# Optimization experiments

Measured on AMD Instinct MI355X. Metric: run time of the kernel, lower is better.

The kernel has to match this reference:

```python
import jax, jax.numpy as jnp
import numpy as np
import math

B, S, D, H = 2, 2048, 1024, 16
HD = D // H  # head dim = 64


def setup_inputs() -> dict:
    key = jax.random.key(0)
    k1, k2, k3, k4, k5 = jax.random.split(key, 5)
    query = jax.random.normal(k1, (B, S, D), dtype=jnp.float32)
    # tail padding: sequence lengths 1536 and 1792 -> positions >= length are padded (True)
    lengths = jnp.array([1536, 1792], dtype=jnp.int32)
    padding_mask = jnp.arange(S, dtype=jnp.int32)[None, :] >= lengths[:, None]  # [B,S] bool
    qkv_w = jax.random.normal(k2, (3 * D, D), dtype=jnp.float32) * 0.02
    qkv_b = jax.random.uniform(k3, (3 * D,), dtype=jnp.float32, minval=-0.03, maxval=0.03)
    out_w = jax.random.normal(k4, (D, D), dtype=jnp.float32) * 0.02
    out_b = jax.random.uniform(k5, (D,), dtype=jnp.float32, minval=-0.03, maxval=0.03)
    return {"query": query, "padding_mask": padding_mask,
            "qkv_w": qkv_w, "qkv_b": qkv_b, "out_w": out_w, "out_b": out_b}


def reference(query, padding_mask, qkv_w, qkv_b, out_w, out_b):
    # self-attention path (qkv_same=True): fused qkv projection then split
    qkv = query @ qkv_w.T + qkv_b                      # [B,S,3D]
    q, k, v = jnp.split(qkv, 3, axis=-1)               # each [B,S,D]

    def split_heads(x):
        return x.reshape(B, S, H, HD).transpose(0, 2, 1, 3)  # [B,H,S,HD]

    q, k, v = split_heads(q), split_heads(k), split_heads(v)

    # scores scaled by sqrt(head_dim)
    w = jnp.einsum('bhqd,bhkd->bhqk', q, k) / math.sqrt(HD)  # [B,H,S,S]

    # causal (future) mask: strict upper triangle masked
    future = jnp.triu(jnp.ones((S, S), dtype=bool), 1)
    w = jnp.where(future[None, None, :, :], -jnp.inf, w)
    # key padding mask
    w = jnp.where(padding_mask[:, None, None, :], -jnp.inf, w)

    a = jax.nn.softmax(w, axis=-1)
    # rows of fully-padded sequences are zeroed (dropout is identity in eval)
    all_masked = jnp.all(padding_mask, axis=-1)        # [B]
    a = jnp.where(all_masked[:, None, None, None], 0.0, a)

    x = jnp.einsum('bhqk,bhkd->bhqd', a, v)            # [B,H,S,HD]
    x = x.transpose(0, 2, 1, 3).reshape(B, S, D)       # merge heads
    return x @ out_w.T + out_b
```

## Files before the change

kernel.cpp:

```cpp
#include <hip/hip_runtime.h>
#include <hip/hip_bf16.h>
#include <stdint.h>

#define S_  2048
#define B_  2
#define H_  16
#define D_  1024
#define HD_ 64

typedef short short8 __attribute__((ext_vector_type(8)));
typedef float f32x4  __attribute__((ext_vector_type(4)));
typedef float f32x16 __attribute__((ext_vector_type(16)));

__device__ __forceinline__ unsigned short bf16_rne(float f) {
  unsigned int u = __float_as_uint(f);
  u += 0x7fffu + ((u >> 16) & 1u);
  return (unsigned short)(u >> 16);
}

__device__ __forceinline__ f32x4 mfma_bf16(short8 a, short8 b, f32x4 c) {
  return __builtin_amdgcn_mfma_f32_16x16x32_bf16(a, b, c, 0, 0, 0);
}

__device__ __forceinline__ f32x16 mfma32(short8 a, short8 b, f32x16 c) {
  return __builtin_amdgcn_mfma_f32_32x32x16_bf16(a, b, c, 0, 0, 0);
}

__device__ __forceinline__ unsigned int cvtpk_bf16(float lo, float hi) {
  unsigned int r;
  asm("v_cvt_pk_bf16_f32 %0, %1, %2" : "=v"(r) : "v"(lo), "v"(hi));
  return r;
}

__global__ void cvt3_kernel(const float* __restrict__ a, unsigned short* __restrict__ oa, int na8,
                            const float* __restrict__ b, unsigned short* __restrict__ ob, int nb8,
                            const float* __restrict__ c, unsigned short* __restrict__ oc, int nc8) {
  int i = blockIdx.x * blockDim.x + threadIdx.x;
  const float* in; unsigned short* out; int idx;
  if (i < na8) { in = a; out = oa; idx = i; }
  else if (i < na8 + nb8) { in = b; out = ob; idx = i - na8; }
  else if (i < na8 + nb8 + nc8) { in = c; out = oc; idx = i - na8 - nb8; }
  else return;
  const float4* p = (const float4*)in + (size_t)idx * 2;
  float4 x = p[0], y = p[1];
  union { unsigned short u[8]; short8 v; } r;
  r.u[0] = bf16_rne(x.x); r.u[1] = bf16_rne(x.y);
  r.u[2] = bf16_rne(x.z); r.u[3] = bf16_rne(x.w);
  r.u[4] = bf16_rne(y.x); r.u[5] = bf16_rne(y.y);
  r.u[6] = bf16_rne(y.z); r.u[7] = bf16_rne(y.w);
  *((short8*)out + idx) = r.v;
}

__global__ void lengths_kernel(const void* __restrict__ mask, int* __restrict__ lens) {
  __shared__ int mn[B_];
  __shared__ int anyb;
  int t = threadIdx.x;
  if (t < B_) mn[t] = S_;
  if (t == 0) anyb = 0;
  __syncthreads();
  const unsigned char* mb = (const unsigned char*)mask;
  for (int i = t; i < B_ * S_; i += 256) {
    if (mb[i]) { anyb = 1; atomicMin(&mn[i >> 11], i & (S_ - 1)); }
  }
  __syncthreads();
  if (!anyb) {
    const int* mi = (const int*)mask;
    for (int i = t; i < B_ * S_; i += 256) {
      if (mi[i]) atomicMin(&mn[i >> 11], i & (S_ - 1));
    }
    __syncthreads();
  }
  if (t < B_) lens[t] = mn[t];
}

__global__ __launch_bounds__(512, 2) void gemm8p_kernel(
    const unsigned short* __restrict__ A,
    const unsigned short* __restrict__ W,
    int K, int NBX,
    const float* __restrict__ bias,
    unsigned short* __restrict__ qb,
    unsigned short* __restrict__ kb,
    unsigned short* __restrict__ vb) {
  __shared__ __align__(16) unsigned short lds[65536];

  const int nwg = gridDim.x;
  const int cpx = nwg >> 3;
  const int bid = blockIdx.x;
  const int virt = (bid & 7) * cpx + (bid >> 3);
  const int bx = virt % NBX, by = virt / NBX;
  const int tile_m = by * 256, tile_n = bx * 256;
  const int t = threadIdx.x;
  const int lane = t & 63, w = t >> 6;
  const int wm = w >> 2, wn = w & 3;
  const int l15 = lane & 15, lk = lane >> 4;
  const int NT = K >> 6;

  f32x4 acc[8][4];
#pragma unroll
  for (int i = 0; i < 8; i++)
#pragma unroll
    for (int j = 0; j < 4; j++) { f32x4 z = {0.f, 0.f, 0.f, 0.f}; acc[i][j] = z; }

  const int L0 = t, L1 = 512 + t;
  const int r0 = L0 >> 3, c0 = (L0 & 7) ^ (r0 & 7);
  const int r1 = L1 >> 3, c1 = (L1 & 7) ^ (r1 & 7);

#define STAGE_HALF(SRC, GROW0, DSTE, KC)                                      \
  {                                                                           \
    __builtin_amdgcn_global_load_lds(                                         \
        (const __attribute__((address_space(1))) void*)(                      \
            (SRC) + (size_t)((GROW0) + r0) * K + (KC) + c0 * 8),              \
        (__attribute__((address_space(3))) void*)(&lds[(DSTE) + L0 * 8]),     \
        16, 0, 0);                                                            \
    __builtin_amdgcn_global_load_lds(                                         \
        (const __attribute__((address_space(1))) void*)(                      \
            (SRC) + (size_t)((GROW0) + r1) * K + (KC) + c1 * 8),              \
        (__attribute__((address_space(3))) void*)(&lds[(DSTE) + L1 * 8]),     \
        16, 0, 0);                                                            \
  }

  STAGE_HALF(A, tile_m,        0,    0);
  STAGE_HALF(W, tile_n,        32768, 0);
  STAGE_HALF(A, tile_m + 128,  8192, 0);
  STAGE_HALF(W, tile_n + 128,  32768 + 8192, 0);
  asm volatile("s_waitcnt vmcnt(4)" ::: "memory");
  __builtin_amdgcn_s_barrier();

  for (int tc = 0; tc < NT; ++tc) {
    const int cb = (tc & 1) * 16384;
    const int ob = ((tc & 1) ^ 1) * 16384;
    int tn = tc + 1; if (tn >= NT) tn = NT - 1;
    const int k0n = tn << 6;

#pragma unroll
    for (int p = 0; p < 4; ++p) {
      const int mh = (p & 1);
      const int nh = (p >> 1);
      short8 af[4][2], bfr[2][2];
#pragma unroll
      for (int fi = 0; fi < 4; ++fi) {
        const int rl = fi * 32 + wm * 16 + l15;
#pragma unroll
        for (int ks = 0; ks < 2; ++ks) {
          const int sw = (ks * 4 + lk) ^ (rl & 7);
          af[fi][ks] = *(const short8*)&lds[cb + mh * 8192 + rl * 64 + sw * 8];
        }
      }
#pragma unroll
      for (int fj = 0; fj < 2; ++fj) {
        const int cl = wn * 32 + fj * 16 + l15;
#pragma unroll
        for (int ks = 0; ks < 2; ++ks) {
          const int sw = (ks * 4 + lk) ^ (cl & 7);
          bfr[fj][ks] =
              *(const short8*)&lds[32768 + cb + nh * 8192 + cl * 64 + sw * 8];
        }
      }
      if (p == 0)      STAGE_HALF(A, tile_m,       ob,                k0n)
      else if (p == 1) STAGE_HALF(W, tile_n,       32768 + ob,        k0n)
      else if (p == 2) STAGE_HALF(A, tile_m + 128, ob + 8192,         k0n)
      else             STAGE_HALF(W, tile_n + 128, 32768 + ob + 8192, k0n);
      if (p != 2) asm volatile("s_waitcnt vmcnt(4)" ::: "memory");
      else        asm volatile("" ::: "memory");
      __builtin_amdgcn_s_barrier();
      asm volatile("s_waitcnt lgkmcnt(0)" ::: "memory");
      __builtin_amdgcn_s_setprio(1);
#pragma unroll
      for (int fi = 0; fi < 4; ++fi)
#pragma unroll
        for (int fj = 0; fj < 2; ++fj)
#pragma unroll
          for (int ks = 0; ks < 2; ++ks)
            acc[mh * 4 + fi][nh * 2 + fj] =
                mfma_bf16(af[fi][ks], bfr[fj][ks], acc[mh * 4 + fi][nh * 2 + fj]);
      __builtin_amdgcn_s_setprio(0);
      __builtin_amdgcn_s_barrier();
    }
  }
  asm volatile("s_waitcnt vmcnt(0)" ::: "memory");
#undef STAGE_HALF

#pragma unroll
  for (int j = 0; j < 4; ++j) {
    const int gn = tile_n + (j >> 1) * 128 + wn * 32 + (j & 1) * 16 + l15;
    const float bv = bias[gn];
    const int which = gn >> 10, dd = gn & (D_ - 1);
    const int h = dd >> 6, d = dd & 63;
    unsigned short* dstp = (which == 0) ? qb : (which == 1) ? kb : vb;
    const float mul = (which == 0) ? 0.125f : 1.0f;
#pragma unroll
    for (int i = 0; i < 8; ++i) {
      const int gmb = tile_m + (i >> 2) * 128 + (i & 3) * 32 + wm * 16 + lk * 4;
#pragma unroll
      for (int r = 0; r < 4; ++r) {
        const int gm = gmb + r;
        const int bb = gm >> 11, s = gm & (S_ - 1);
        dstp[((size_t)((bb * H_ + h) * S_ + s)) * HD_ + d] =
            bf16_rne((acc[i][j][r] + bv) * mul);
      }
    }
  }
}

__global__ __launch_bounds__(256) void gemm_bt_kernel(
    const unsigned short* __restrict__ A,
    const unsigned short* __restrict__ W,
    int K, int N,
    const float* __restrict__ bias,
    float* __restrict__ outf) {
  __shared__ unsigned short As[128 * 32];
  __shared__ unsigned short Bs[128 * 32];
  const int tile_m = blockIdx.y * 128;
  const int tile_n = blockIdx.x * 128;
  const int t = threadIdx.x;
  const int lane = t & 63;
  const int w = t >> 6;
  const int wr = w >> 1, wc = w & 1;
  const int l15 = lane & 15, lk = lane >> 4;

  f32x4 acc[4][4];
#pragma unroll
  for (int i = 0; i < 4; i++)
#pragma unroll
    for (int j = 0; j < 4; j++) { f32x4 z = {0.f, 0.f, 0.f, 0.f}; acc[i][j] = z; }

  for (int k0 = 0; k0 < K; k0 += 32) {
#pragma unroll
    for (int c = 0; c < 2; ++c) {
      int e = (c * 256 + t) * 8;
      int row = e >> 5, col = e & 31;
      __builtin_amdgcn_global_load_lds(
          (__attribute__((address_space(1))) void*)(A + (size_t)(tile_m + row) * K + k0 + col),
          (__attribute__((address_space(3))) void*)(&As[e]), 16, 0, 0);
      __builtin_amdgcn_global_load_lds(
          (__attribute__((address_space(1))) void*)(W + (size_t)(tile_n + row) * K + k0 + col),
          (__attribute__((address_space(3))) void*)(&Bs[e]), 16, 0, 0);
    }
    asm volatile("s_waitcnt vmcnt(0)" ::: "memory");
    __syncthreads();

    short8 af[4], bfr[4];
#pragma unroll
    for (int i = 0; i < 4; i++)
      af[i] = *(const short8*)&As[(wr * 64 + i * 16 + l15) * 32 + lk * 8];
#pragma unroll
    for (int j = 0; j < 4; j++)
      bfr[j] = *(const short8*)&Bs[(wc * 64 + j * 16 + l15) * 32 + lk * 8];
#pragma unroll
    for (int i = 0; i < 4; i++)
#pragma unroll
      for (int j = 0; j < 4; j++)
        acc[i][j] = mfma_bf16(af[i], bfr[j], acc[i][j]);
    __syncthreads();
  }

#pragma unroll
  for (int i = 0; i < 4; i++) {
#pragma unroll
    for (int j = 0; j < 4; j++) {
      int gn = tile_n + wc * 64 + j * 16 + l15;
      float bv = bias[gn];
#pragma unroll
      for (int r = 0; r < 4; r++) {
        int gm = tile_m + wr * 64 + i * 16 + lk * 4 + r;
        outf[(size_t)gm * N + gn] = acc[i][j][r] + bv;
      }
    }
  }
}

__global__ __launch_bounds__(256, 3) void attn_kernel(
    const unsigned short* __restrict__ qbuf,
    const unsigned short* __restrict__ kbuf,
    const unsigned short* __restrict__ vbuf,
    const int* __restrict__ lens,
    unsigned short* __restrict__ attn_out) {
  __shared__ __align__(16) char smem[33792];
  __shared__ float lsh[2][64];

  const int bid = blockIdx.x;
  const int virt = ((bid & 7) << 7) | (bid >> 3);
  const int bh = virt >> 5;
  const int qt = virt & 31;
  const int b = bh >> 4;
  const int len = lens[b];
  const int t = threadIdx.x;
  const int lane = t & 63, w = t >> 6;
  const int g = w >> 1, wq = w & 1;
  const int l31 = lane & 31, hi = lane >> 5;
  const int hi8 = hi * 8, hi4 = hi * 4;
  const int q0 = qt * 64 + wq * 32;
  const int qme = q0 + l31;

  unsigned short* Ks = (unsigned short*)(smem + g * 8192);
  unsigned int*   Vt = (unsigned int*)(smem + 16384 + g * 8704);

  const unsigned short* qbh = qbuf + (size_t)bh * S_ * HD_;
  const unsigned short* kbh = kbuf + (size_t)bh * S_ * HD_;
  const unsigned short* vbh = vbuf + (size_t)bh * S_ * HD_;

  short8 qf[4];
#pragma unroll
  for (int ds = 0; ds < 4; ++ds)
    qf[ds] = *(const short8*)&qbh[(size_t)(q0 + l31) * HD_ + ds * 16 + hi8];

  f32x16 o[2] = {{}, {}};
  float rsum = 0.f;

  const int ke = (len - 1) >> 6;
  const int kt_end = qt < ke ? qt : ke;
  const int NI = (kt_end >> 1) + 1;

  const int tg = t & 127;
  const int kr0 = tg >> 3, kc0 = tg & 7;
  const int vr2 = tg & 31, vcb = (tg >> 5) << 1;

  short8 pk[4], pva0 = {}, pva1 = {}, pvb0 = {}, pvb1 = {};
#pragma unroll
  for (int m = 0; m < 4; ++m) pk[m] = pva0;

#define LDG(KT)                                                               \
  {                                                                           \
    int ks_ = (KT) * 64;                                                      \
    pk[0] = *(const short8*)&kbh[(size_t)(ks_ + kr0     ) * HD_ + kc0 * 8];   \
    pk[1] = *(const short8*)&kbh[(size_t)(ks_ + kr0 + 16) * HD_ + kc0 * 8];   \
    pk[2] = *(const short8*)&kbh[(size_t)(ks_ + kr0 + 32) * HD_ + kc0 * 8];   \
    pk[3] = *(const short8*)&kbh[(size_t)(ks_ + kr0 + 48) * HD_ + kc0 * 8];   \
    const unsigned short* vp = vbh + (size_t)(ks_ + 2 * vr2) * HD_ + vcb * 8; \
    pva0 = *(const short8*)vp;       pva1 = *(const short8*)(vp + HD_);       \
    pvb0 = *(const short8*)(vp + 8); pvb1 = *(const short8*)(vp + HD_ + 8);   \
  }

  int my_kt = g;
  bool act = (my_kt <= kt_end);
  if (act) LDG(my_kt);

  typedef union { unsigned int u[4]; short8 s; } pa_t;

  for (int i = 0; i < NI; ++i) {
    __syncthreads();
    if (act) {
#pragma unroll
      for (int m = 0; m < 4; ++m) {
        const int r = kr0 + 16 * m;
        *(short8*)&Ks[r * 64 + ((kc0 ^ (r & 7)) << 3)] = pk[m];
      }
#pragma unroll
      for (int j = 0; j < 8; ++j) {
        unsigned int w0 = (unsigned int)(unsigned short)pva0[j] |
                          ((unsigned int)(unsigned short)pva1[j] << 16);
        unsigned int w1 = (unsigned int)(unsigned short)pvb0[j] |
                          ((unsigned int)(unsigned short)pvb1[j] << 16);
        Vt[(vcb * 8 + j) * 34 + vr2] = w0;
        Vt[((vcb + 1) * 8 + j) * 34 + vr2] = w1;
      }
    }
    __syncthreads();
    const int nxt = my_kt + 2;
    const bool nact = (nxt <= kt_end);
    if (nact) LDG(nxt);

    const int ks0 = my_kt * 64;
    if (act && ks0 <= q0 + 31) {
      const bool needM = (ks0 + 63 >= q0) || (ks0 + 63 >= len);
      const bool dokb1 = (ks0 + 32 <= q0 + 31) && (ks0 + 32 < len);

      pa_t pa[4];
      {
        f32x16 s0 = {};
#pragma unroll
        for (int ds = 0; ds < 4; ++ds) {
          const int cg = ((ds << 1) | hi) ^ (l31 & 7);
          const short8 kf = *(const short8*)&Ks[l31 * 64 + (cg << 3)];
          s0 = mfma32(kf, qf[ds], s0);
        }
        float pr[16];
#pragma unroll
        for (int r = 0; r < 16; ++r) {
          const int crow = (r & 3) + 8 * (r >> 2) + hi4;
          float p = __expf(s0[r]);
          if (needM) {
            const int key = ks0 + crow;
            if (key > qme || key >= len) p = 0.f;
          }
          pr[r] = p; rsum += p;
        }
        unsigned int A0 = cvtpk_bf16(pr[0], pr[1]);
        unsigned int A1 = cvtpk_bf16(pr[2], pr[3]);
        unsigned int B0 = cvtpk_bf16(pr[4], pr[5]);
        unsigned int B1 = cvtpk_bf16(pr[6], pr[7]);
        asm volatile("v_permlane32_swap_b32 %0, %1" : "+v"(A0), "+v"(B0));
        asm volatile("v_permlane32_swap_b32 %0, %1" : "+v"(A1), "+v"(B1));
        pa[0].u[0] = A0; pa[0].u[1] = A1; pa[0].u[2] = B0; pa[0].u[3] = B1;
        unsigned int C0 = cvtpk_bf16(pr[8], pr[9]);
        unsigned int C1 = cvtpk_bf16(pr[10], pr[11]);
        unsigned int D0 = cvtpk_bf16(pr[12], pr[13]);
        unsigned int D1 = cvtpk_bf16(pr[14], pr[15]);
        asm volatile("v_permlane32_swap_b32 %0, %1" : "+v"(C0), "+v"(D0));
        asm volatile("v_permlane32_swap_b32 %0, %1" : "+v"(C1), "+v"(D1));
        pa[1].u[0] = C0; pa[1].u[1] = C1; pa[1].u[2] = D0; pa[1].u[3] = D1;
      }
      if (dokb1) {
        f32x16 s1 = {};
#pragma unroll
        for (int ds = 0; ds < 4; ++ds) {
          const int cg = ((ds << 1) | hi) ^ (l31 & 7);
          const short8 kf = *(const short8*)&Ks[(32 + l31) * 64 + (cg << 3)];
          s1 = mfma32(kf, qf[ds], s1);
        }
        float pr[16];
#pragma unroll
        for (int r = 0; r < 16; ++r) {
          const int crow = 32 + (r & 3) + 8 * (r >> 2) + hi4;
          float p = __expf(s1[r]);
          if (needM) {
            const int key = ks0 + crow;
            if (key > qme || key >= len) p = 0.f;
          }
          pr[r] = p; rsum += p;
        }
        unsigned int A0 = cvtpk_bf16(pr[0], pr[1]);
        unsigned int A1 = cvtpk_bf16(pr[2], pr[3]);
        unsigned int B0 = cvtpk_bf16(pr[4], pr[5]);
        unsigned int B1 = cvtpk_bf16(pr[6], pr[7]);
        asm volatile("v_permlane32_swap_b32 %0, %1" : "+v"(A0), "+v"(B0));
        asm volatile("v_permlane32_swap_b32 %0, %1" : "+v"(A1), "+v"(B1));
        pa[2].u[0] = A0; pa[2].u[1] = A1; pa[2].u[2] = B0; pa[2].u[3] = B1;
        unsigned int C0 = cvtpk_bf16(pr[8], pr[9]);
        unsigned int C1 = cvtpk_bf16(pr[10], pr[11]);
        unsigned int D0 = cvtpk_bf16(pr[12], pr[13]);
        unsigned int D1 = cvtpk_bf16(pr[14], pr[15]);
        asm volatile("v_permlane32_swap_b32 %0, %1" : "+v"(C0), "+v"(D0));
        asm volatile("v_permlane32_swap_b32 %0, %1" : "+v"(C1), "+v"(D1));
        pa[3].u[0] = C0; pa[3].u[1] = C1; pa[3].u[2] = D0; pa[3].u[3] = D1;
      }
#pragma unroll
      for (int dh = 0; dh < 2; ++dh) {
        const int vbase = (dh * 32 + l31) * 34 + hi4;
#pragma unroll
        for (int ks = 0; ks < 4; ++ks) {
          if (ks >= 2 && !dokb1) continue;
          uint2 va = *(const uint2*)&Vt[vbase + 8 * ks];
          uint2 vb2 = *(const uint2*)&Vt[vbase + 8 * ks + 2];
          pa_t vv;
          vv.u[0] = va.x; vv.u[1] = va.y; vv.u[2] = vb2.x; vv.u[3] = vb2.y;
          o[dh] = mfma32(pa[ks].s, vv.s, o[dh]);
        }
      }
    }
    my_kt = nxt; act = nact;
  }
#undef LDG

  rsum += __shfl_xor(rsum, 32, 64);

  float* mo = (float*)smem;
  __syncthreads();
  if (g == 1) {
#pragma unroll
    for (int r = 0; r < 16; ++r) {
      const int qb = wq * 32 + (r & 3) + 8 * (r >> 2) + hi4;
      mo[qb * 66 + l31]      = o[0][r];
      mo[qb * 66 + 32 + l31] = o[1][r];
    }
    if (hi == 0) lsh[1][wq * 32 + l31] = rsum;
  }
  __syncthreads();
  if (g == 0) {
    const float lt = rsum + lsh[1][wq * 32 + l31];
    const float inv = (lt > 0.f) ? (1.0f / lt) : 0.f;
    if (hi == 0) lsh[0][wq * 32 + l31] = inv;
#pragma unroll
    for (int r = 0; r < 16; ++r) {
      const int cr = (r & 3) + 8 * (r >> 2) + hi4;
      const int qb = wq * 32 + cr;
      const float iv = lsh[0][wq * 32 + cr];
      const int s = qt * 64 + qb;
      unsigned short* op =
          &attn_out[((size_t)(b * S_ + s)) * D_ + (bh & 15) * HD_ + l31];
      op[0]  = bf16_rne((o[0][r] + mo[qb * 66 + l31]) * iv);
      op[32] = bf16_rne((o[1][r] + mo[qb * 66 + 32 + l31]) * iv);
    }
  }
}

extern "C" void kernel_launch(void* const* d_in, const int* in_sizes, int n_in,
                              void* d_out, int out_size, void* d_ws, size_t ws_size,
                              hipStream_t stream) {
  const float* query = (const float*)d_in[0];
  const void*  mask  = d_in[1];
  const float* qkv_w = (const float*)d_in[2];
  const float* qkv_b = (const float*)d_in[3];
  const float* out_w = (const float*)d_in[4];
  const float* out_b = (const float*)d_in[5];
  float* out = (float*)d_out;

  char* ws = (char*)d_ws;
  unsigned short* qx     = (unsigned short*)(ws);
  unsigned short* wqkv   = (unsigned short*)(ws + (8u  << 20));
  unsigned short* wout   = (unsigned short*)(ws + (14u << 20));
  unsigned short* qbuf   = (unsigned short*)(ws + (16u << 20));
  unsigned short* kbuf   = (unsigned short*)(ws + (24u << 20));
  unsigned short* vbuf   = (unsigned short*)(ws + (32u << 20));
  unsigned short* attn_o = qx;
  int* lens              = (int*)(ws + (40u << 20));

  lengths_kernel<<<1, 256, 0, stream>>>(mask, lens);
  const int na8 = B_ * S_ * D_ / 8, nb8 = 3 * D_ * D_ / 8, nc8 = D_ * D_ / 8;
  cvt3_kernel<<<(na8 + nb8 + nc8) / 256, 256, 0, stream>>>(
      query, qx, na8, qkv_w, wqkv, nb8, out_w, wout, nc8);

  gemm8p_kernel<<<192, 512, 0, stream>>>(qx, wqkv, D_, 3 * D_ / 256, qkv_b,
                                         qbuf, kbuf, vbuf);

  attn_kernel<<<1024, 256, 0, stream>>>(qbuf, kbuf, vbuf, lens, attn_o);

  dim3 g2(D_ / 128, B_ * S_ / 128);
  gemm_bt_kernel<<<g2, 256, 0, stream>>>(attn_o, wout, D_, D_, out_b, out);
}
```

Before: 144.0 us.

## Pre-transpose V and use LDS-free single-wave attention blocks

Adds a separate kernel that transposes V into a [bh, d, s] layout. Attention then runs one 64-thread wave per 32-query tile, loading K and transposed V fragments straight from global memory instead of staging them in shared memory. This removes the LDS writes, the barriers and the cross-wave reduction of partial outputs and row sums. In exchange it adds an extra launch and a full pass over V, loses K/V reuse between waves, and each wave now walks its whole key range alone, which lengthens the critical path for late query tiles.

```diff
diff --git a/kernel.cpp b/kernel.cpp
--- a/kernel.cpp
+++ b/kernel.cpp
@@ -202,6 +202,30 @@
   }
 }
 
+__global__ __launch_bounds__(256) void vtrans_kernel(
+    const unsigned short* __restrict__ v, unsigned short* __restrict__ vt) {
+  __shared__ unsigned short tile[64][66];
+  const int bid = blockIdx.x;
+  const int bh = bid >> 5, st = bid & 31;
+  const int t = threadIdx.x;
+  const int r = t >> 2, c = (t & 3) * 16;
+  const unsigned short* src = v + ((size_t)bh * S_ + st * 64) * HD_;
+  short8 a0 = *(const short8*)&src[r * HD_ + c];
+  short8 a1 = *(const short8*)&src[r * HD_ + c + 8];
+  *(short8*)&tile[r][c] = a0;
+  *(short8*)&tile[r][c + 8] = a1;
+  __syncthreads();
+  union { unsigned short u[8]; short8 v8; } o0, o1;
+#pragma unroll
+  for (int j = 0; j < 8; ++j) {
+    o0.u[j] = tile[c + j][r];
+    o1.u[j] = tile[c + 8 + j][r];
+  }
+  unsigned short* dst = vt + ((size_t)bh * HD_ + r) * S_ + st * 64 + c;
+  *(short8*)dst = o0.v8;
+  *(short8*)(dst + 8) = o1.v8;
+}
+
 __global__ __launch_bounds__(256) void gemm_bt_kernel(
     const unsigned short* __restrict__ A,
     const unsigned short* __restrict__ W,
@@ -269,35 +293,27 @@
   }
 }
 
-__global__ __launch_bounds__(256, 3) void attn_kernel(
+__global__ __launch_bounds__(64) void attn_kernel(
     const unsigned short* __restrict__ qbuf,
     const unsigned short* __restrict__ kbuf,
-    const unsigned short* __restrict__ vbuf,
+    const unsigned short* __restrict__ vtbuf,
     const int* __restrict__ lens,
     unsigned short* __restrict__ attn_out) {
-  __shared__ __align__(16) char smem[33792];
-  __shared__ float lsh[2][64];
-
   const int bid = blockIdx.x;
-  const int virt = ((bid & 7) << 7) | (bid >> 3);
-  const int bh = virt >> 5;
-  const int qt = virt & 31;
+  const int virt = ((bid & 7) << 8) | (bid >> 3);
+  const int bh = virt >> 6;
+  const int qs = 63 - (virt & 63);
   const int b = bh >> 4;
   const int len = lens[b];
-  const int t = threadIdx.x;
-  const int lane = t & 63, w = t >> 6;
-  const int g = w >> 1, wq = w & 1;
+  const int lane = threadIdx.x & 63;
   const int l31 = lane & 31, hi = lane >> 5;
   const int hi8 = hi * 8, hi4 = hi * 4;
-  const int q0 = qt * 64 + wq * 32;
+  const int q0 = qs * 32;
   const int qme = q0 + l31;
-
-  unsigned short* Ks = (unsigned short*)(smem + g * 8192);
-  unsigned int*   Vt = (unsigned int*)(smem + 16384 + g * 8704);
 
   const unsigned short* qbh = qbuf + (size_t)bh * S_ * HD_;
   const unsigned short* kbh = kbuf + (size_t)bh * S_ * HD_;
-  const unsigned short* vbh = vbuf + (size_t)bh * S_ * HD_;
+  const unsigned short* vth = vtbuf + (size_t)bh * HD_ * S_;
 
   short8 qf[4];
 #pragma unroll
@@ -307,180 +323,111 @@
   f32x16 o[2] = {{}, {}};
   float rsum = 0.f;
 
-  const int ke = (len - 1) >> 6;
-  const int kt_end = qt < ke ? qt : ke;
-  const int NI = (kt_end >> 1) + 1;
-
-  const int tg = t & 127;
-  const int kr0 = tg >> 3, kc0 = tg & 7;
-  const int vr2 = tg & 31, vcb = (tg >> 5) << 1;
-
-  short8 pk[4], pva0 = {}, pva1 = {}, pvb0 = {}, pvb1 = {};
-#pragma unroll
-  for (int m = 0; m < 4; ++m) pk[m] = pva0;
-
-#define LDG(KT)                                                               \
-  {                                                                           \
-    int ks_ = (KT) * 64;                                                      \
-    pk[0] = *(const short8*)&kbh[(size_t)(ks_ + kr0     ) * HD_ + kc0 * 8];   \
-    pk[1] = *(const short8*)&kbh[(size_t)(ks_ + kr0 + 16) * HD_ + kc0 * 8];   \
-    pk[2] = *(const short8*)&kbh[(size_t)(ks_ + kr0 + 32) * HD_ + kc0 * 8];   \
-    pk[3] = *(const short8*)&kbh[(size_t)(ks_ + kr0 + 48) * HD_ + kc0 * 8];   \
-    const unsigned short* vp = vbh + (size_t)(ks_ + 2 * vr2) * HD_ + vcb * 8; \
-    pva0 = *(const short8*)vp;       pva1 = *(const short8*)(vp + HD_);       \
-    pvb0 = *(const short8*)(vp + 8); pvb1 = *(const short8*)(vp + HD_ + 8);   \
-  }
-
-  int my_kt = g;
-  bool act = (my_kt <= kt_end);
-  if (act) LDG(my_kt);
+  const int lastk = (q0 + 31 < len - 1) ? (q0 + 31) : (len - 1);
+  const int kt_end = lastk >> 6;
 
   typedef union { unsigned int u[4]; short8 s; } pa_t;
 
-  for (int i = 0; i < NI; ++i) {
-    __syncthreads();
-    if (act) {
-#pragma unroll
-      for (int m = 0; m < 4; ++m) {
-        const int r = kr0 + 16 * m;
-        *(short8*)&Ks[r * 64 + ((kc0 ^ (r & 7)) << 3)] = pk[m];
-      }
-#pragma unroll
-      for (int j = 0; j < 8; ++j) {
-        unsigned int w0 = (unsigned int)(unsigned short)pva0[j] |
-                          ((unsigned int)(unsigned short)pva1[j] << 16);
-        unsigned int w1 = (unsigned int)(unsigned short)pvb0[j] |
-                          ((unsigned int)(unsigned short)pvb1[j] << 16);
-        Vt[(vcb * 8 + j) * 34 + vr2] = w0;
-        Vt[((vcb + 1) * 8 + j) * 34 + vr2] = w1;
-      }
-    }
-    __syncthreads();
-    const int nxt = my_kt + 2;
-    const bool nact = (nxt <= kt_end);
-    if (nact) LDG(nxt);
-
-    const int ks0 = my_kt * 64;
-    if (act && ks0 <= q0 + 31) {
+  for (int kt = 0; kt <= kt_end; ++kt) {
+    const int ks0 = kt * 64;
+    const bool dokb1 = (ks0 + 32 <= lastk);
+    pa_t pa[4];
+
+    {
+      f32x16 s0 = {};
+#pragma unroll
+      for (int ds = 0; ds < 4; ++ds) {
+        const short8 kf =
+            *(const short8*)&kbh[(size_t)(ks0 + l31) * HD_ + ds * 16 + hi8];
+        s0 = mfma32(kf, qf[ds], s0);
+      }
+      const bool needM = (ks0 + 31 >= q0) || (ks0 + 31 >= len);
+      float pr[16];
+#pragma unroll
+      for (int r = 0; r < 16; ++r) {
+        const int crow = (r & 3) + 8 * (r >> 2) + hi4;
+        float p = __expf(s0[r]);
+        if (needM) {
+          const int key = ks0 + crow;
+          if (key > qme || key >= len) p = 0.f;
+        }
+        pr[r] = p; rsum += p;
+      }
+      unsigned int A0 = cvtpk_bf16(pr[0], pr[1]);
+      unsigned int A1 = cvtpk_bf16(pr[2], pr[3]);
+      unsigned int B0 = cvtpk_bf16(pr[4], pr[5]);
+      unsigned int B1 = cvtpk_bf16(pr[6], pr[7]);
+      asm volatile("v_permlane32_swap_b32 %0, %1" : "+v"(A0), "+v"(B0));
+      asm volatile("v_permlane32_swap_b32 %0, %1" : "+v"(A1), "+v"(B1));
+      pa[0].u[0] = A0; pa[0].u[1] = A1; pa[0].u[2] = B0; pa[0].u[3] = B1;
+      unsigned int C0 = cvtpk_bf16(pr[8], pr[9]);
+      unsigned int C1 = cvtpk_bf16(pr[10], pr[11]);
+      unsigned int D0 = cvtpk_bf16(pr[12], pr[13]);
+      unsigned int D1 = cvtpk_bf16(pr[14], pr[15]);
+      asm volatile("v_permlane32_swap_b32 %0, %1" : "+v"(C0), "+v"(D0));
+      asm volatile("v_permlane32_swap_b32 %0, %1" : "+v"(C1), "+v"(D1));
+      pa[1].u[0] = C0; pa[1].u[1] = C1; pa[1].u[2] = D0; pa[1].u[3] = D1;
+    }
+    if (dokb1) {
+      f32x16 s1 = {};
+#pragma unroll
+      for (int ds = 0; ds < 4; ++ds) {
+        const short8 kf =
+            *(const short8*)&kbh[(size_t)(ks0 + 32 + l31) * HD_ + ds * 16 + hi8];
+        s1 = mfma32(kf, qf[ds], s1);
+      }
       const bool needM = (ks0 + 63 >= q0) || (ks0 + 63 >= len);
-      const bool dokb1 = (ks0 + 32 <= q0 + 31) && (ks0 + 32 < len);
-
-      pa_t pa[4];
-      {
-        f32x16 s0 = {};
-#pragma unroll
-        for (int ds = 0; ds < 4; ++ds) {
-          const int cg = ((ds << 1) | hi) ^ (l31 & 7);
-          const short8 kf = *(const short8*)&Ks[l31 * 64 + (cg << 3)];
-          s0 = mfma32(kf, qf[ds], s0);
+      float pr[16];
+#pragma unroll
+      for (int r = 0; r < 16; ++r) {
+        const int crow = 32 + (r & 3) + 8 * (r >> 2) + hi4;
+        float p = __expf(s1[r]);
+        if (needM) {
+          const int key = ks0 + crow;
+          if (key > qme || key >= len) p = 0.f;
         }
-        float pr[16];
-#pragma unroll
-        for (int r = 0; r < 16; ++r) {
-          const int crow = (r & 3) + 8 * (r >> 2) + hi4;
-          float p = __expf(s0[r]);
-          if (needM) {
-            const int key = ks0 + crow;
-            if (key > qme || key >= len) p = 0.f;
-          }
-          pr[r] = p; rsum += p;
-        }
-        unsigned int A0 = cvtpk_bf16(pr[0], pr[1]);
-        unsigned int A1 = cvtpk_bf16(pr[2], pr[3]);
-        unsigned int B0 = cvtpk_bf16(pr[4], pr[5]);
-        unsigned int B1 = cvtpk_bf16(pr[6], pr[7]);
-        asm volatile("v_permlane32_swap_b32 %0, %1" : "+v"(A0), "+v"(B0));
-        asm volatile("v_permlane32_swap_b32 %0, %1" : "+v"(A1), "+v"(B1));
-        pa[0].u[0] = A0; pa[0].u[1] = A1; pa[0].u[2] = B0; pa[0].u[3] = B1;
-        unsigned int C0 = cvtpk_bf16(pr[8], pr[9]);
-        unsigned int C1 = cvtpk_bf16(pr[10], pr[11]);
-        unsigned int D0 = cvtpk_bf16(pr[12], pr[13]);
-        unsigned int D1 = cvtpk_bf16(pr[14], pr[15]);
-        asm volatile("v_permlane32_swap_b32 %0, %1" : "+v"(C0), "+v"(D0));
-        asm volatile("v_permlane32_swap_b32 %0, %1" : "+v"(C1), "+v"(D1));
-        pa[1].u[0] = C0; pa[1].u[1] = C1; pa[1].u[2] = D0; pa[1].u[3] = D1;
-      }
-      if (dokb1) {
-        f32x16 s1 = {};
-#pragma unroll
-        for (int ds = 0; ds < 4; ++ds) {
-          const int cg = ((ds << 1) | hi) ^ (l31 & 7);
-          const short8 kf = *(const short8*)&Ks[(32 + l31) * 64 + (cg << 3)];
-          s1 = mfma32(kf, qf[ds], s1);
-        }
-        float pr[16];
-#pragma unroll
-        for (int r = 0; r < 16; ++r) {
-          const int crow = 32 + (r & 3) + 8 * (r >> 2) + hi4;
-          float p = __expf(s1[r]);
-          if (needM) {
-            const int key = ks0 + crow;
-            if (key > qme || key >= len) p = 0.f;
-          }
-          pr[r] = p; rsum += p;
-        }
-        unsigned int A0 = cvtpk_bf16(pr[0], pr[1]);
-        unsigned int A1 = cvtpk_bf16(pr[2], pr[3]);
-        unsigned int B0 = cvtpk_bf16(pr[4], pr[5]);
-        unsigned int B1 = cvtpk_bf16(pr[6], pr[7]);
-        asm volatile("v_permlane32_swap_b32 %0, %1" : "+v"(A0), "+v"(B0));
-        asm volatile("v_permlane32_swap_b32 %0, %1" : "+v"(A1), "+v"(B1));
-        pa[2].u[0] = A0; pa[2].u[1] = A1; pa[2].u[2] = B0; pa[2].u[3] = B1;
-        unsigned int C0 = cvtpk_bf16(pr[8], pr[9]);
-        unsigned int C1 = cvtpk_bf16(pr[10], pr[11]);
-        unsigned int D0 = cvtpk_bf16(pr[12], pr[13]);
-        unsigned int D1 = cvtpk_bf16(pr[14], pr[15]);
-        asm volatile("v_permlane32_swap_b32 %0, %1" : "+v"(C0), "+v"(D0));
-        asm volatile("v_permlane32_swap_b32 %0, %1" : "+v"(C1), "+v"(D1));
-        pa[3].u[0] = C0; pa[3].u[1] = C1; pa[3].u[2] = D0; pa[3].u[3] = D1;
-      }
-#pragma unroll
-      for (int dh = 0; dh < 2; ++dh) {
-        const int vbase = (dh * 32 + l31) * 34 + hi4;
-#pragma unroll
-        for (int ks = 0; ks < 4; ++ks) {
-          if (ks >= 2 && !dokb1) continue;
-          uint2 va = *(const uint2*)&Vt[vbase + 8 * ks];
-          uint2 vb2 = *(const uint2*)&Vt[vbase + 8 * ks + 2];
-          pa_t vv;
-          vv.u[0] = va.x; vv.u[1] = va.y; vv.u[2] = vb2.x; vv.u[3] = vb2.y;
-          o[dh] = mfma32(pa[ks].s, vv.s, o[dh]);
-        }
-      }
-    }
-    my_kt = nxt; act = nact;
-  }
-#undef LDG
+        pr[r] = p; rsum += p;
+      }
+      unsigned int A0 = cvtpk_bf16(pr[0], pr[1]);
+      unsigned int A1 = cvtpk_bf16(pr[2], pr[3]);
+      unsigned int B0 = cvtpk_bf16(pr[4], pr[5]);
+      unsigned int B1 = cvtpk_bf16(pr[6], pr[7]);
+      asm volatile("v_permlane32_swap_b32 %0, %1" : "+v"(A0), "+v"(B0));
+      asm volatile("v_permlane32_swap_b32 %0, %1" : "+v"(A1), "+v"(B1));
+      pa[2].u[0] = A0; pa[2].u[1] = A1; pa[2].u[2] = B0; pa[2].u[3] = B1;
+      unsigned int C0 = cvtpk_bf16(pr[8], pr[9]);
+      unsigned int C1 = cvtpk_bf16(pr[10], pr[11]);
+      unsigned int D0 = cvtpk_bf16(pr[12], pr[13]);
+      unsigned int D1 = cvtpk_bf16(pr[14], pr[15]);
+      asm volatile("v_permlane32_swap_b32 %0, %1" : "+v"(C0), "+v"(D0));
+      asm volatile("v_permlane32_swap_b32 %0, %1" : "+v"(C1), "+v"(D1));
+      pa[3].u[0] = C0; pa[3].u[1] = C1; pa[3].u[2] = D0; pa[3].u[3] = D1;
+    }
+#pragma unroll
+    for (int dh = 0; dh < 2; ++dh) {
+      const unsigned short* vrow =
+          &vth[(size_t)(dh * 32 + l31) * S_ + ks0 + hi8];
+#pragma unroll
+      for (int c = 0; c < 4; ++c) {
+        if (c >= 2 && !dokb1) continue;
+        const short8 vv = *(const short8*)&vrow[c * 16];
+        o[dh] = mfma32(pa[c].s, vv, o[dh]);
+      }
+    }
+  }
 
   rsum += __shfl_xor(rsum, 32, 64);
-
-  float* mo = (float*)smem;
-  __syncthreads();
-  if (g == 1) {
-#pragma unroll
-    for (int r = 0; r < 16; ++r) {
-      const int qb = wq * 32 + (r & 3) + 8 * (r >> 2) + hi4;
-      mo[qb * 66 + l31]      = o[0][r];
-      mo[qb * 66 + 32 + l31] = o[1][r];
-    }
-    if (hi == 0) lsh[1][wq * 32 + l31] = rsum;
-  }
-  __syncthreads();
-  if (g == 0) {
-    const float lt = rsum + lsh[1][wq * 32 + l31];
-    const float inv = (lt > 0.f) ? (1.0f / lt) : 0.f;
-    if (hi == 0) lsh[0][wq * 32 + l31] = inv;
-#pragma unroll
-    for (int r = 0; r < 16; ++r) {
-      const int cr = (r & 3) + 8 * (r >> 2) + hi4;
-      const int qb = wq * 32 + cr;
-      const float iv = lsh[0][wq * 32 + cr];
-      const int s = qt * 64 + qb;
-      unsigned short* op =
-          &attn_out[((size_t)(b * S_ + s)) * D_ + (bh & 15) * HD_ + l31];
-      op[0]  = bf16_rne((o[0][r] + mo[qb * 66 + l31]) * iv);
-      op[32] = bf16_rne((o[1][r] + mo[qb * 66 + 32 + l31]) * iv);
-    }
+  const float inv = (rsum > 0.f) ? (1.0f / rsum) : 0.f;
+
+#pragma unroll
+  for (int r = 0; r < 16; ++r) {
+    const int crow = (r & 3) + 8 * (r >> 2) + hi4;
+    const float iv = __shfl(inv, crow, 64);
+    const int s = q0 + crow;
+    unsigned short* op =
+        &attn_out[((size_t)(b * S_ + s)) * D_ + (bh & 15) * HD_ + l31];
+    op[0]  = bf16_rne(o[0][r] * iv);
+    op[32] = bf16_rne(o[1][r] * iv);
   }
 }
 
@@ -498,11 +445,12 @@
   char* ws = (char*)d_ws;
   unsigned short* qx     = (unsigned short*)(ws);
   unsigned short* wqkv   = (unsigned short*)(ws + (8u  << 20));
+  unsigned short* vtbuf  = (unsigned short*)(ws + (6u  << 20));
   unsigned short* wout   = (unsigned short*)(ws + (14u << 20));
   unsigned short* qbuf   = (unsigned short*)(ws + (16u << 20));
   unsigned short* kbuf   = (unsigned short*)(ws + (24u << 20));
   unsigned short* vbuf   = (unsigned short*)(ws + (32u << 20));
-  unsigned short* attn_o = qx;
+  unsigned short* attn_o = vbuf;
   int* lens              = (int*)(ws + (40u << 20));
 
   lengths_kernel<<<1, 256, 0, stream>>>(mask, lens);
@@ -513,7 +461,9 @@
   gemm8p_kernel<<<192, 512, 0, stream>>>(qx, wqkv, D_, 3 * D_ / 256, qkv_b,
                                          qbuf, kbuf, vbuf);
 
-  attn_kernel<<<1024, 256, 0, stream>>>(qbuf, kbuf, vbuf, lens, attn_o);
+  vtrans_kernel<<<1024, 256, 0, stream>>>(vbuf, vtbuf);
+
+  attn_kernel<<<2048, 64, 0, stream>>>(qbuf, kbuf, vtbuf, lens, attn_o);
 
   dim3 g2(D_ / 128, B_ * S_ / 128);
   gemm_bt_kernel<<<g2, 256, 0, stream>>>(attn_o, wout, D_, D_, out_b, out);
```

Result: slower. 181.1 us (+25.8%).

## Split attention KV range into chunks with atomic merge and exp2 scaling

Applied to the files above, without the earlier changes.

Splits each query tile's key range into chunks of 8 key tiles, so later (longer) query tiles are spread over several blocks, and the grid grows from 1024 to 2560 blocks. Partial unnormalized outputs and row sums go to fp32 buffers through atomicAdd, and a new merge kernel normalizes them to bf16. Q is prescaled by log2(e)/8 so exp2f can replace __expf. The cost is extra memsets, atomic traffic and one more launch. The kernel still uses no running max, so it relies on scores staying small enough for exp2 not to overflow.

```diff
diff --git a/kernel.cpp b/kernel.cpp
--- a/kernel.cpp
+++ b/kernel.cpp
@@ -187,7 +187,7 @@
     const int which = gn >> 10, dd = gn & (D_ - 1);
     const int h = dd >> 6, d = dd & 63;
     unsigned short* dstp = (which == 0) ? qb : (which == 1) ? kb : vb;
-    const float mul = (which == 0) ? 0.125f : 1.0f;
+    const float mul = (which == 0) ? 0.18033688011112042f : 1.0f;
 #pragma unroll
     for (int i = 0; i < 8; ++i) {
       const int gmb = tile_m + (i >> 2) * 128 + (i & 3) * 32 + wm * 16 + lk * 4;
@@ -274,14 +274,21 @@
     const unsigned short* __restrict__ kbuf,
     const unsigned short* __restrict__ vbuf,
     const int* __restrict__ lens,
-    unsigned short* __restrict__ attn_out) {
+    unsigned short* __restrict__ attn_out,
+    float* __restrict__ oacc,
+    float* __restrict__ lacc) {
   __shared__ __align__(16) char smem[33792];
   __shared__ float lsh[2][64];
 
   const int bid = blockIdx.x;
-  const int virt = ((bid & 7) << 7) | (bid >> 3);
-  const int bh = virt >> 5;
-  const int qt = virt & 31;
+  const int xcd = bid & 7, idx = bid >> 3;
+  const int bh = (xcd << 2) | (idx & 3);
+  const int cid = idx >> 2;
+  const int m = (cid < 8) ? 0 : (cid < 24) ? 1 : (cid < 48) ? 2 : 3;
+  const int cbase = 4 * m * (m + 1);
+  const int qt = 8 * m + (cid - cbase) / (m + 1);
+  const int chunk = (cid - cbase) % (m + 1);
+  const int nch = m + 1;
   const int b = bh >> 4;
   const int len = lens[b];
   const int t = threadIdx.x;
@@ -309,7 +316,10 @@
 
   const int ke = (len - 1) >> 6;
   const int kt_end = qt < ke ? qt : ke;
-  const int NI = (kt_end >> 1) + 1;
+  const int k0t = chunk * 8;
+  const int klast = (k0t + 7 < kt_end) ? (k0t + 7) : kt_end;
+  const int count = klast - k0t + 1;
+  const int NI = (count + 1) >> 1;
 
   const int tg = t & 127;
   const int kr0 = tg >> 3, kc0 = tg & 7;
@@ -317,7 +327,7 @@
 
   short8 pk[4], pva0 = {}, pva1 = {}, pvb0 = {}, pvb1 = {};
 #pragma unroll
-  for (int m = 0; m < 4; ++m) pk[m] = pva0;
+  for (int mm = 0; mm < 4; ++mm) pk[mm] = pva0;
 
 #define LDG(KT)                                                               \
   {                                                                           \
@@ -331,8 +341,8 @@
     pvb0 = *(const short8*)(vp + 8); pvb1 = *(const short8*)(vp + HD_ + 8);   \
   }
 
-  int my_kt = g;
-  bool act = (my_kt <= kt_end);
+  int my_kt = k0t + g;
+  bool act = (my_kt <= klast);
   if (act) LDG(my_kt);
 
   typedef union { unsigned int u[4]; short8 s; } pa_t;
@@ -341,9 +351,9 @@
     __syncthreads();
     if (act) {
 #pragma unroll
-      for (int m = 0; m < 4; ++m) {
-        const int r = kr0 + 16 * m;
-        *(short8*)&Ks[r * 64 + ((kc0 ^ (r & 7)) << 3)] = pk[m];
+      for (int mm = 0; mm < 4; ++mm) {
+        const int r = kr0 + 16 * mm;
+        *(short8*)&Ks[r * 64 + ((kc0 ^ (r & 7)) << 3)] = pk[mm];
       }
 #pragma unroll
       for (int j = 0; j < 8; ++j) {
@@ -357,7 +367,7 @@
     }
     __syncthreads();
     const int nxt = my_kt + 2;
-    const bool nact = (nxt <= kt_end);
+    const bool nact = (nxt <= klast);
     if (nact) LDG(nxt);
 
     const int ks0 = my_kt * 64;
@@ -378,7 +388,7 @@
 #pragma unroll
         for (int r = 0; r < 16; ++r) {
           const int crow = (r & 3) + 8 * (r >> 2) + hi4;
-          float p = __expf(s0[r]);
+          float p = exp2f(s0[r]);
           if (needM) {
             const int key = ks0 + crow;
             if (key > qme || key >= len) p = 0.f;
@@ -412,7 +422,7 @@
 #pragma unroll
         for (int r = 0; r < 16; ++r) {
           const int crow = 32 + (r & 3) + 8 * (r >> 2) + hi4;
-          float p = __expf(s1[r]);
+          float p = exp2f(s1[r]);
           if (needM) {
             const int key = ks0 + crow;
             if (key > qme || key >= len) p = 0.f;
@@ -467,21 +477,54 @@
   }
   __syncthreads();
   if (g == 0) {
-    const float lt = rsum + lsh[1][wq * 32 + l31];
-    const float inv = (lt > 0.f) ? (1.0f / lt) : 0.f;
-    if (hi == 0) lsh[0][wq * 32 + l31] = inv;
-#pragma unroll
-    for (int r = 0; r < 16; ++r) {
-      const int cr = (r & 3) + 8 * (r >> 2) + hi4;
-      const int qb = wq * 32 + cr;
-      const float iv = lsh[0][wq * 32 + cr];
-      const int s = qt * 64 + qb;
-      unsigned short* op =
-          &attn_out[((size_t)(b * S_ + s)) * D_ + (bh & 15) * HD_ + l31];
-      op[0]  = bf16_rne((o[0][r] + mo[qb * 66 + l31]) * iv);
-      op[32] = bf16_rne((o[1][r] + mo[qb * 66 + 32 + l31]) * iv);
-    }
-  }
+    const int myrow = wq * 32 + l31;
+    const float lt = rsum + lsh[1][myrow];
+    if (nch == 1) {
+      const float inv = (lt > 0.f) ? (1.0f / lt) : 0.f;
+      if (hi == 0) lsh[0][myrow] = inv;
+#pragma unroll
+      for (int r = 0; r < 16; ++r) {
+        const int cr = (r & 3) + 8 * (r >> 2) + hi4;
+        const int qb = wq * 32 + cr;
+        const float iv = lsh[0][qb];
+        const int s = qt * 64 + qb;
+        unsigned short* op =
+            &attn_out[((size_t)(b * S_ + s)) * D_ + (bh & 15) * HD_ + l31];
+        op[0]  = bf16_rne((o[0][r] + mo[qb * 66 + l31]) * iv);
+        op[32] = bf16_rne((o[1][r] + mo[qb * 66 + 32 + l31]) * iv);
+      }
+    } else {
+      if (hi == 0) atomicAdd(&lacc[(bh << 11) + qt * 64 + myrow], lt);
+#pragma unroll
+      for (int r = 0; r < 16; ++r) {
+        const int cr = (r & 3) + 8 * (r >> 2) + hi4;
+        const int qb = wq * 32 + cr;
+        const int s = qt * 64 + qb;
+        float* oa = &oacc[((size_t)(b * S_ + s)) * D_ + (bh & 15) * HD_ + l31];
+        atomicAdd(oa,      o[0][r] + mo[qb * 66 + l31]);
+        atomicAdd(oa + 32, o[1][r] + mo[qb * 66 + 32 + l31]);
+      }
+    }
+  }
+}
+
+__global__ __launch_bounds__(256) void attn_merge_kernel(
+    const float* __restrict__ oacc, const float* __restrict__ lacc,
+    unsigned short* __restrict__ attn_out) {
+  const int q = blockIdx.x * 256 + threadIdx.x;
+  const int b = q / 393216;
+  const int rem = q - b * 393216;
+  const int s = 512 + (rem >> 8);
+  const int hd = rem & 255;
+  const int h = hd >> 4, dq = hd & 15;
+  const float l = lacc[((b * 16 + h) << 11) + s];
+  const float inv = (l > 0.f) ? (1.0f / l) : 0.f;
+  const size_t off = ((size_t)(b * S_ + s)) * D_ + h * HD_ + dq * 4;
+  const float4 v = *(const float4*)&oacc[off];
+  union { unsigned short u[4]; uint2 v2; } r;
+  r.u[0] = bf16_rne(v.x * inv); r.u[1] = bf16_rne(v.y * inv);
+  r.u[2] = bf16_rne(v.z * inv); r.u[3] = bf16_rne(v.w * inv);
+  *(uint2*)&attn_out[off] = r.v2;
 }
 
 extern "C" void kernel_launch(void* const* d_in, const int* in_sizes, int n_in,
@@ -503,9 +546,12 @@
   unsigned short* kbuf   = (unsigned short*)(ws + (24u << 20));
   unsigned short* vbuf   = (unsigned short*)(ws + (32u << 20));
   unsigned short* attn_o = qx;
+  float* lacc            = (float*)(ws + (8u << 20));
+  float* oacc            = out;
   int* lens              = (int*)(ws + (40u << 20));
 
   lengths_kernel<<<1, 256, 0, stream>>>(mask, lens);
+  hipMemsetAsync(d_out, 0, (size_t)B_ * S_ * D_ * 4, stream);
   const int na8 = B_ * S_ * D_ / 8, nb8 = 3 * D_ * D_ / 8, nc8 = D_ * D_ / 8;
   cvt3_kernel<<<(na8 + nb8 + nc8) / 256, 256, 0, stream>>>(
       query, qx, na8, qkv_w, wqkv, nb8, out_w, wout, nc8);
@@ -513,7 +559,11 @@
   gemm8p_kernel<<<192, 512, 0, stream>>>(qx, wqkv, D_, 3 * D_ / 256, qkv_b,
                                          qbuf, kbuf, vbuf);
 
-  attn_kernel<<<1024, 256, 0, stream>>>(qbuf, kbuf, vbuf, lens, attn_o);
+  hipMemsetAsync(lacc, 0, 32 * 2048 * 4, stream);
+
+  attn_kernel<<<2560, 256, 0, stream>>>(qbuf, kbuf, vbuf, lens, attn_o,
+                                        oacc, lacc);
+  attn_merge_kernel<<<3072, 256, 0, stream>>>(oacc, lacc, attn_o);
 
   dim3 g2(D_ / 128, B_ * S_ / 128);
   gemm_bt_kernel<<<g2, 256, 0, stream>>>(attn_o, wout, D_, D_, out_b, out);
```

After: 153.0 us. 1.06x slower.
